# Kernel tuning notes

Measured on AMD Instinct MI355X. Metric: run time of the kernel, lower is better.

## Reference

```python
import jax, jax.numpy as jnp
import numpy as np

B, CIN, H, W = 32, 512, 16, 16
COUT, HEADS, SPARSITY = 2048, 8, 7
D = COUT // HEADS  # 256, must equal H*W
N = H * W


def conv1x1(x, w, b):
    # x: [B,C,H,W], w: [O,C], b: [O]
    return jnp.einsum('bchw,oc->bohw', x, w) + b[None, :, None, None]


def setup_inputs() -> dict:
    key = jax.random.key(0)
    ks = jax.random.split(key, 11)
    def lin(k, o, c):
        bound = 1.0 / np.sqrt(c)
        kw, kb = jax.random.split(k)
        return (jax.random.uniform(kw, (o, c), jnp.float32, -bound, bound),
                jax.random.uniform(kb, (o,), jnp.float32, -bound, bound))
    Wq, bq = lin(ks[0], COUT, CIN)
    Wk, bk = lin(ks[1], COUT, CIN)
    Wv, bv = lin(ks[2], COUT, CIN)
    Wo, bo = lin(ks[3], COUT, COUT)
    # kaiming_uniform_ on [COUT, COUT]
    gain = np.sqrt(2.0) / np.sqrt(5.0)  # default a=sqrt(5)
    bound = gain * np.sqrt(3.0 / COUT)
    coeff = jax.random.uniform(ks[4], (COUT, COUT), jnp.float32, -bound, bound)
    scale = jnp.array([np.sqrt(D)], jnp.float32)
    x = jax.random.normal(ks[5], (B, CIN, H, W), jnp.float32)
    return {"x": x, "Wq": Wq, "bq": bq, "Wk": Wk, "bk": bk, "Wv": Wv,
            "bv": bv, "Wo": Wo, "bo": bo, "coeff": coeff, "scale": scale}


def reference(x, Wq, bq, Wk, bk, Wv, bv, Wo, bo, coeff, scale):
    # enforce_sparsity: keep top-`SPARSITY` |coeff| per row, zero the rest
    _, idx = jax.lax.top_k(jnp.abs(coeff), SPARSITY)  # [COUT, SPARSITY]
    mask = jnp.zeros(coeff.shape, bool).at[jnp.arange(COUT)[:, None], idx].set(True)
    coeff_s = jnp.where(mask, coeff, 0.0)

    q = conv1x1(x, Wq, bq).reshape(B, HEADS, D, N)
    k = conv1x1(x, Wk, bk).reshape(B, HEADS, D, N)
    v = conv1x1(x, Wv, bv).reshape(B, HEADS, D, N)

    attn = jnp.einsum('bhdn,bhdm->bhnm', q, k) / scale[0]  # [B,h,N,N]
    sparse_attn = jnp.einsum('bhnm,mp->bhnp', attn, coeff_s[:D, :D])
    sparse_attn = jax.nn.softmax(sparse_attn, axis=-1)
    out = jnp.einsum('bhnm,bhmd->bhnd', sparse_attn, v.transpose(0, 1, 3, 2))
    out = out.transpose(0, 1, 3, 2).reshape(B, COUT, H, W)
    return conv1x1(out, Wo, bo)
```

## Files before the change

kernel.cpp:

```cpp
#include <hip/hip_runtime.h>

typedef unsigned short ushort;
typedef __attribute__((ext_vector_type(8))) short short8;
typedef __attribute__((ext_vector_type(8))) unsigned short ushort8;
typedef __attribute__((ext_vector_type(4))) unsigned short ushort4v;
typedef __attribute__((ext_vector_type(4))) float fx4;

#define MAXNNZ (256*7)

__device__ __forceinline__ ushort f2bf(float f) {
    union { float f; unsigned u; } v; v.f = f;
    unsigned r = v.u + 0x7fffu + ((v.u >> 16) & 1u);
    return (ushort)(r >> 16);
}

__device__ __forceinline__ float bf2f(ushort b) {
    union { unsigned u; float f; } v; v.u = ((unsigned)b) << 16;
    return v.f;
}

__device__ __forceinline__ void gload_lds16(const ushort* g, ushort* l) {
    __builtin_amdgcn_global_load_lds(
        (const __attribute__((address_space(1))) unsigned int*)g,
        (__attribute__((address_space(3))) unsigned int*)l, 16, 0, 0);
}

__global__ __launch_bounds__(256)
void topk_kernel(const float* __restrict__ coeff,
                 int* __restrict__ coo_cnt, int* __restrict__ coo_m,
                 int* __restrict__ coo_p, float* __restrict__ coo_v)
{
    int row = blockIdx.x;
    int tid = threadIdx.x;
    const float* crow = coeff + (long)row * 2048;
    float av[8];
#pragma unroll
    for (int i = 0; i < 8; ++i) av[i] = fabsf(crow[tid + 256 * i]);
    __shared__ unsigned long long red[256];
    for (int t = 0; t < 7; ++t) {
        float mx = -1.f; int mi = 0;
#pragma unroll
        for (int i = 0; i < 8; ++i) if (av[i] > mx) { mx = av[i]; mi = i; }
        unsigned col = (unsigned)(tid + 256 * mi);
        unsigned long long pk = ((unsigned long long)__float_as_uint(mx) << 32)
                              | (unsigned long long)(2048u - col);
        red[tid] = pk; __syncthreads();
        for (int s = 128; s > 0; s >>= 1) {
            if (tid < s) { if (red[tid + s] > red[tid]) red[tid] = red[tid + s]; }
            __syncthreads();
        }
        unsigned long long w = red[0];
        __syncthreads();
        unsigned wcol = 2048u - (unsigned)(w & 0xffffffffu);
        if ((wcol & 255u) == (unsigned)tid) av[wcol >> 8] = -1.f;
        if (tid == 0 && wcol < 256u) {
            int pos = atomicAdd(coo_cnt, 1);
            coo_m[pos] = row; coo_p[pos] = (int)wcol; coo_v[pos] = crow[wcol];
        }
    }
}

__global__ __launch_bounds__(256)
void csc_kernel(const int* __restrict__ coo_cnt, const int* __restrict__ coo_m,
                const int* __restrict__ coo_p, const float* __restrict__ coo_v,
                int* __restrict__ csc_ptr, int* __restrict__ csc_m,
                float* __restrict__ csc_v, float* __restrict__ csum)
{
    __shared__ int cnt[256];
    __shared__ int off[257];
    __shared__ int cur[256];
    int tid = threadIdx.x;
    cnt[tid] = 0;
    __syncthreads();
    int n = *coo_cnt; if (n > MAXNNZ) n = MAXNNZ;
    for (int e = tid; e < n; e += 256) atomicAdd(&cnt[coo_p[e]], 1);
    __syncthreads();
    if (tid == 0) {
        int s = 0;
        for (int p = 0; p < 256; ++p) { off[p] = s; s += cnt[p]; }
        off[256] = s;
    }
    __syncthreads();
    csc_ptr[tid] = off[tid];
    if (tid == 0) csc_ptr[256] = off[256];
    cur[tid] = off[tid];
    __syncthreads();
    for (int e = tid; e < n; e += 256) {
        int p = coo_p[e];
        int pos = atomicAdd(&cur[p], 1);
        csc_m[pos] = coo_m[e];
        csc_v[pos] = coo_v[e];
    }
    __syncthreads();
    {
        float s = 0.f;
        int e0 = off[tid], e1 = off[tid] + cnt[tid];
        for (int e = e0; e < e1; ++e) s += csc_v[e];
        csum[tid] = s;
    }
}

__global__ void cvt4_kernel(const float* a0, ushort* d0, int n0,
                            const float* a1, ushort* d1, int n1,
                            const float* a2, ushort* d2, int n2,
                            const float* a3, ushort* d3, int n3)
{
    const float* s; ushort* d; int n;
    switch (blockIdx.y) {
        case 0: s = a0; d = d0; n = n0; break;
        case 1: s = a1; d = d1; n = n1; break;
        case 2: s = a2; d = d2; n = n2; break;
        default: s = a3; d = d3; n = n3; break;
    }
    int nv = n >> 2;
    for (int i = blockIdx.x * blockDim.x + threadIdx.x; i < nv; i += gridDim.x * blockDim.x) {
        fx4 v = ((const fx4*)s)[i];
        ushort4v o;
        o[0] = f2bf(v[0]); o[1] = f2bf(v[1]); o[2] = f2bf(v[2]); o[3] = f2bf(v[3]);
        ((ushort4v*)d)[i] = o;
    }
}

__global__ __launch_bounds__(256)
void transpose_f32_bf16(const float* __restrict__ in, ushort* __restrict__ out, int R, int C)
{
    int z = blockIdx.z;
    const float* ib = in + (long)z * R * C;
    ushort* ob = out + (long)z * R * C;
    __shared__ ushort tile[64][72];
    int r0 = blockIdx.x * 64, c0 = blockIdx.y * 64;
    int tid = threadIdx.x;
    int rl = tid >> 2, sg = tid & 3;
#pragma unroll
    for (int h = 0; h < 4; ++h) {
        fx4 v = *(const fx4*)(ib + (long)(r0 + rl) * C + c0 + h * 16 + sg * 4);
#pragma unroll
        for (int i = 0; i < 4; ++i) tile[h * 16 + sg * 4 + i][rl] = f2bf(v[i]);
    }
    __syncthreads();
    int cl = rl;
#pragma unroll
    for (int h = 0; h < 2; ++h) {
        ushort8 vv = *(const ushort8*)(&tile[cl][h * 32 + sg * 8]);
        *(ushort8*)(ob + (long)(c0 + cl) * R + r0 + h * 32 + sg * 8) = vv;
    }
}

__global__ __launch_bounds__(256)
void xcomb_kernel(const ushort* __restrict__ xT, ushort* __restrict__ xc,
                  const int* __restrict__ csc_ptr, const int* __restrict__ csc_m,
                  const float* __restrict__ csc_v)
{
    int b = blockIdx.y;
    int tid = threadIdx.x;
    int p = blockIdx.x * 32 + (tid >> 3);
    int c0 = (tid & 7) * 64;
    const ushort* src = xT + (long)b * 131072;
    float acc[64];
#pragma unroll
    for (int i = 0; i < 64; ++i) acc[i] = 0.f;
    int e0 = csc_ptr[p], e1 = csc_ptr[p + 1];
    for (int e = e0; e < e1; ++e) {
        const ushort* row = src + csc_m[e] * 512 + c0;
        float c = csc_v[e];
#pragma unroll
        for (int u = 0; u < 8; ++u) {
            ushort8 v = *(const ushort8*)(row + u * 8);
#pragma unroll
            for (int t = 0; t < 8; ++t) acc[u * 8 + t] += bf2f(v[t]) * c;
        }
    }
    ushort* dst = xc + (long)b * 131072 + (long)p * 512 + c0;
#pragma unroll
    for (int u = 0; u < 8; ++u) {
        ushort8 o;
#pragma unroll
        for (int t = 0; t < 8; ++t) o[t] = f2bf(acc[u * 8 + t]);
        *(ushort8*)(dst + u * 8) = o;
    }
}

__global__ __launch_bounds__(256, 2)
void attn_kernel(const ushort* __restrict__ Q, const ushort* __restrict__ Kt,
                 const ushort* __restrict__ V, ushort* __restrict__ O,
                 const float* __restrict__ scale_src)
{
    __shared__ __align__(16) ushort PQ[32768];
    __shared__ float rmax[4][128];
    __shared__ float rsum[4][128];

    int bid = blockIdx.x;
    int hf = bid >> 8, z = bid & 255;
    int b = z >> 3, h = z & 7;
    const ushort* Qz = Q + (long)z * 65536 + (long)hf * 32768;
    const ushort* Kz = Kt + (long)z * 65536;
    const ushort* Vz = V + (long)b * 524288 + (long)h * 65536;
    ushort* Ob = O + (long)b * 524288 + (long)h * 256 + (long)hf * 128 * 2048;

    int tid = threadIdx.x;
    int wave = tid >> 6, lane = tid & 63;
    int l16 = lane & 15, quad = lane >> 4;
    int key = l16 & 7;

    {
        int rb = wave * 2 + (lane >> 5);
        const ushort* qsrc = Qz + (long)rb * 256 + (((lane & 31) ^ (rb & 7)) * 8);
        ushort* qdst = PQ + wave * 512;
#pragma unroll
        for (int g = 0; g < 16; ++g)
            gload_lds16(qsrc + g * 2048, qdst + g * 2048);
    }

    const ushort* kfp = Kz + (long)(wave * 64 + l16) * 256 + quad * 8;
    const ushort* vfp = Vz + (long)(wave * 64 + l16) * 256 + quad * 8;

    fx4 acc[8][4];
#pragma unroll
    for (int i = 0; i < 8; ++i)
#pragma unroll
        for (int j = 0; j < 4; ++j) acc[i][j] = (fx4){0.f, 0.f, 0.f, 0.f};

    short8 bfn[4];
#pragma unroll
    for (int j = 0; j < 4; ++j) bfn[j] = *(const short8*)(kfp + j * 4096);

    __syncthreads();

    float sc = 1.0f / scale_src[0];

#pragma unroll
    for (int kd = 0; kd < 8; ++kd) {
        short8 bf[4];
#pragma unroll
        for (int j = 0; j < 4; ++j) bf[j] = bfn[j];
        if (kd < 7) {
#pragma unroll
            for (int j = 0; j < 4; ++j)
                bfn[j] = *(const short8*)(kfp + j * 4096 + (kd + 1) * 32);
        }
        short8 af[8];
#pragma unroll
        for (int i = 0; i < 8; ++i)
            af[i] = *(const short8*)(PQ + (i * 16 + l16) * 256 + (((kd * 4 + quad) ^ key) * 8));
        __builtin_amdgcn_s_setprio(1);
#pragma unroll
        for (int i = 0; i < 8; ++i)
#pragma unroll
            for (int j = 0; j < 4; ++j)
                acc[i][j] = __builtin_amdgcn_mfma_f32_16x16x32_bf16(af[i], bf[j], acc[i][j], 0, 0, 0);
        __builtin_amdgcn_s_setprio(0);
    }

#pragma unroll
    for (int i = 0; i < 8; ++i)
#pragma unroll
        for (int j = 0; j < 4; ++j)
#pragma unroll
            for (int r = 0; r < 4; ++r) acc[i][j][r] *= sc;

    float lm[8][4];
#pragma unroll
    for (int i = 0; i < 8; ++i)
#pragma unroll
        for (int r = 0; r < 4; ++r) {
            float m = -1e30f;
#pragma unroll
            for (int j = 0; j < 4; ++j) m = fmaxf(m, acc[i][j][r]);
            lm[i][r] = m;
        }
#pragma unroll
    for (int d = 1; d < 16; d <<= 1)
#pragma unroll
        for (int i = 0; i < 8; ++i)
#pragma unroll
            for (int r = 0; r < 4; ++r) lm[i][r] = fmaxf(lm[i][r], __shfl_xor(lm[i][r], d, 16));
    if (l16 == 0) {
#pragma unroll
        for (int i = 0; i < 8; ++i)
#pragma unroll
            for (int r = 0; r < 4; ++r)
                rmax[wave][i * 16 + quad * 4 + r] = lm[i][r];
    }
    __syncthreads();

    float ls[8][4];
#pragma unroll
    for (int i = 0; i < 8; ++i)
#pragma unroll
        for (int r = 0; r < 4; ++r) {
            int row = i * 16 + quad * 4 + r;
            float M = fmaxf(fmaxf(rmax[0][row], rmax[1][row]),
                            fmaxf(rmax[2][row], rmax[3][row]));
            float s = 0.f;
#pragma unroll
            for (int j = 0; j < 4; ++j) {
                float e = __expf(acc[i][j][r] - M);
                acc[i][j][r] = e;
                s += e;
            }
            ls[i][r] = s;
        }
#pragma unroll
    for (int d = 1; d < 16; d <<= 1)
#pragma unroll
        for (int i = 0; i < 8; ++i)
#pragma unroll
            for (int r = 0; r < 4; ++r) ls[i][r] += __shfl_xor(ls[i][r], d, 16);
    if (l16 == 0) {
#pragma unroll
        for (int i = 0; i < 8; ++i)
#pragma unroll
            for (int r = 0; r < 4; ++r)
                rsum[wave][i * 16 + quad * 4 + r] = ls[i][r];
    }
    __syncthreads();

    short8 vfn[4];
#pragma unroll
    for (int j = 0; j < 4; ++j) vfn[j] = *(const short8*)(vfp + j * 4096);

#pragma unroll
    for (int i = 0; i < 8; ++i)
#pragma unroll
        for (int r = 0; r < 4; ++r) {
            int row = i * 16 + quad * 4 + r;
            float inv = 1.0f / (rsum[0][row] + rsum[1][row] + rsum[2][row] + rsum[3][row]);
            int k2 = row & 7;
#pragma unroll
            for (int j = 0; j < 4; ++j) {
                int p = wave * 64 + j * 16 + l16;
                PQ[row * 256 + ((((p >> 3) ^ k2) << 3) | (p & 7))] = f2bf(acc[i][j][r] * inv);
            }
        }
    __syncthreads();

    fx4 acc2[8][4];
#pragma unroll
    for (int i = 0; i < 8; ++i)
#pragma unroll
        for (int j = 0; j < 4; ++j) acc2[i][j] = (fx4){0.f, 0.f, 0.f, 0.f};

#pragma unroll
    for (int kp = 0; kp < 8; ++kp) {
        short8 vf[4];
#pragma unroll
        for (int j = 0; j < 4; ++j) vf[j] = vfn[j];
        if (kp < 7) {
#pragma unroll
            for (int j = 0; j < 4; ++j)
                vfn[j] = *(const short8*)(vfp + j * 4096 + (kp + 1) * 32);
        }
        short8 pa[8];
#pragma unroll
        for (int i = 0; i < 8; ++i)
            pa[i] = *(const short8*)(PQ + (i * 16 + l16) * 256 + (((kp * 4 + quad) ^ key) * 8));
        __builtin_amdgcn_s_setprio(1);
#pragma unroll
        for (int i = 0; i < 8; ++i)
#pragma unroll
            for (int j = 0; j < 4; ++j)
                acc2[i][j] = __builtin_amdgcn_mfma_f32_16x16x32_bf16(pa[i], vf[j], acc2[i][j], 0, 0, 0);
        __builtin_amdgcn_s_setprio(0);
    }

    __syncthreads();
#pragma unroll
    for (int i = 0; i < 8; ++i)
#pragma unroll
        for (int j = 0; j < 4; ++j) {
            int rowb = i * 16 + quad * 4;
            int col = wave * 64 + j * 16 + l16;
#pragma unroll
            for (int rr = 0; rr < 4; ++rr) {
                int row = rowb + rr;
                PQ[row * 256 + ((((col >> 3) ^ (row & 7)) << 3) | (col & 7))]
                    = f2bf(acc2[i][j][rr]);
            }
        }
    __syncthreads();
#pragma unroll
    for (int pass = 0; pass < 16; ++pass) {
        int row = pass * 8 + (tid >> 5), ch = tid & 31;
        ushort8 vv = *(const ushort8*)(PQ + row * 256 + ((ch ^ (row & 7)) << 3));
        *(ushort8*)(Ob + (long)row * 2048 + ch * 8) = vv;
    }
}

template<int MODE>
__global__ __launch_bounds__(512, 2)
void gemm256(const ushort* __restrict__ A, const ushort* __restrict__ B,
             const ushort* __restrict__ B2, void* __restrict__ C,
             ushort* __restrict__ Kout,
             const float* __restrict__ bias0, const float* __restrict__ bias1,
             const float* __restrict__ bias2, const float* __restrict__ csum,
             int MT, int K)
{
    __shared__ __align__(16) ushort lds[4][2][8192];

    int nwg = gridDim.x;
    int bid = blockIdx.x;
    int mt, nt;
    if (MODE == 4) {
        int xcd = bid & 7, idx = bid >> 3;
        mt = (xcd & 1) * 12 + idx % 12;
        nt = (xcd >> 1) * 8 + idx / 12;
    } else {
        int cpx = nwg >> 3;
        int swz = (bid & 7) * cpx + (bid >> 3);
        mt = swz % MT; nt = swz / MT;
    }
    int m0 = mt << 8, n0 = nt << 8;
    int sec = m0 >> 11;

    int tid = threadIdx.x;
    int wave = tid >> 6, lane = tid & 63;
    int wr = wave >> 2, wc = wave & 3;
    int l16 = lane & 15, quad = lane >> 4;

    const ushort* Bb = (MODE == 4 && sec == 1) ? B2 : B;

    int lc = (((lane & 3) ^ ((lane >> 3) & 3))) * 8;
    const ushort* gA0 = A + (long long)(m0 + wave * 16 + (lane >> 2)) * K + lc;
    const ushort* gA1 = gA0 + (long long)128 * K;
    const ushort* gB0 = Bb + (long long)(n0 + wave * 16 + (lane >> 2)) * K + lc;
    const ushort* gB1 = gB0 + (long long)128 * K;
    int ldso = wave * 512;

    int rsw = ((l16 >> 1) & 3) * 8;
    int aoff = (wr * 128 + l16) * 32 + ((quad * 8) ^ rsw);
    int boff = (wc * 64 + l16) * 32 + ((quad * 8) ^ rsw);

    fx4 acc[8][4];
#pragma unroll
    for (int i = 0; i < 8; ++i)
#pragma unroll
        for (int j = 0; j < 4; ++j) acc[i][j] = (fx4){0.f, 0.f, 0.f, 0.f};

    auto stageA = [&](int b, int kc) {
        gload_lds16(gA0 + kc, &lds[b][0][ldso]);
        gload_lds16(gA1 + kc, &lds[b][0][4096 + ldso]);
    };
    auto stageB = [&](int b, int kc) {
        gload_lds16(gB0 + kc, &lds[b][1][ldso]);
        gload_lds16(gB1 + kc, &lds[b][1][4096 + ldso]);
    };

    short8 af[4], bf[4];
    auto readA = [&](int b, int half) {
        const ushort* p = &lds[b][0][aoff + half * 2048];
#pragma unroll
        for (int i = 0; i < 4; ++i) af[i] = *(const short8*)(p + i * 512);
    };
    auto readB = [&](int b) {
        const ushort* p = &lds[b][1][boff];
#pragma unroll
        for (int j = 0; j < 4; ++j) bf[j] = *(const short8*)(p + j * 512);
    };
    auto mma = [&](int half) {
        __builtin_amdgcn_s_setprio(1);
#pragma unroll
        for (int i = 0; i < 4; ++i)
#pragma unroll
            for (int j = 0; j < 4; ++j)
                acc[half * 4 + i][j] =
                    __builtin_amdgcn_mfma_f32_16x16x32_bf16(af[i], bf[j], acc[half * 4 + i][j], 0, 0, 0);
        __builtin_amdgcn_s_setprio(0);
    };

    int NT = K >> 5;
    stageA(0, 0);  stageB(0, 0);
    stageA(1, 32); stageB(1, 32);
    stageA(2, 64); stageB(2, 64);
    asm volatile("s_waitcnt vmcnt(8)" ::: "memory");
    __builtin_amdgcn_s_barrier();

    for (int t = 0; t < NT; ++t) {
        int b = t & 3;
        readA(b, 0); readB(b);
        if (t + 3 < NT) stageA((t + 3) & 3, (t + 3) << 5);
        __builtin_amdgcn_s_barrier();
        asm volatile("s_waitcnt lgkmcnt(0)" ::: "memory");
        __builtin_amdgcn_sched_barrier(0);
        mma(0);
        __builtin_amdgcn_s_barrier();
        readA(b, 1);
        if (t + 3 < NT) {
            stageB((t + 3) & 3, (t + 3) << 5);
            asm volatile("s_waitcnt vmcnt(8)" ::: "memory");
        } else if (t + 2 < NT) {
            asm volatile("s_waitcnt vmcnt(4)" ::: "memory");
        } else if (t + 1 < NT) {
            asm volatile("s_waitcnt vmcnt(0)" ::: "memory");
        }
        __builtin_amdgcn_s_barrier();
        asm volatile("s_waitcnt lgkmcnt(0)" ::: "memory");
        __builtin_amdgcn_sched_barrier(0);
        mma(1);
        __builtin_amdgcn_s_barrier();
    }

    if (MODE == 5) {
        float* Cf = (float*)C + (long long)nt * 524288;
#pragma unroll
        for (int i = 0; i < 8; ++i) {
            int m = m0 + wr * 128 + i * 16 + quad * 4;
#pragma unroll
            for (int j = 0; j < 4; ++j) {
                int n = wc * 64 + j * 16 + l16;
                float* dst = Cf + (long long)m * 256 + n;
#pragma unroll
                for (int r = 0; r < 4; ++r)
                    dst[(long)r * 256] = acc[i][j][r] + bias0[m + r];
            }
        }
        return;
    }

    if (MODE == 4) {
        int ms0 = m0 & 2047;
        ushort* ct = &lds[0][0][0];
        if (sec < 2) {
            const float* bs = (sec == 0) ? bias0 : bias1;
            ushort* base = ((sec == 0) ? (ushort*)C : Kout)
                         + (long long)nt * 524288 + (long long)(ms0 >> 8) * 65536;
#pragma unroll
            for (int hh = 0; hh < 2; ++hh) {
                if ((wc >> 1) == hh) {
#pragma unroll
                    for (int i = 0; i < 8; ++i)
#pragma unroll
                        for (int j = 0; j < 4; ++j) {
                            int nl = (wc & 1) * 64 + j * 16 + l16;
                            int ml = wr * 128 + i * 16 + quad * 4;
                            float csf = (sec == 1) ? csum[hh * 128 + nl] : 1.0f;
                            ushort4v pk;
#pragma unroll
                            for (int r = 0; r < 4; ++r)
                                pk[r] = f2bf(acc[i][j][r] + bs[ms0 + ml + r] * csf);
                            *(ushort4v*)(ct + nl * 264 + ml) = pk;
                        }
                }
                __syncthreads();
                int row = tid & 127, c0 = (tid >> 7) * 64;
                ushort* dst = base + (long long)(hh * 128 + row) * 256 + c0;
                const ushort* src = ct + row * 264 + c0;
#pragma unroll
                for (int u = 0; u < 8; ++u)
                    *(ushort8*)(dst + u * 8) = *(const ushort8*)(src + u * 8);
                __syncthreads();
            }
        } else {
            ushort* base = (ushort*)C + 33554432LL + (long long)nt * 524288
                         + (long long)ms0 * 256;
#pragma unroll
            for (int hh = 0; hh < 2; ++hh) {
                if (wr == hh) {
#pragma unroll
                    for (int i = 0; i < 8; ++i)
#pragma unroll
                        for (int j = 0; j < 4; ++j) {
                            int nl = wc * 64 + j * 16 + l16;
                            int ml = i * 16 + quad * 4;
#pragma unroll
                            for (int r = 0; r < 4; ++r)
                                ct[(ml + r) * 264 + nl] =
                                    f2bf(acc[i][j][r] + bias2[ms0 + hh * 128 + ml + r]);
                        }
                }
                __syncthreads();
                int row = tid & 127, c0 = (tid >> 7) * 64;
                ushort* dst = base + (long long)(hh * 128 + row) * 256 + c0;
                const ushort* src = ct + row * 264 + c0;
#pragma unroll
                for (int u = 0; u < 8; ++u)
                    *(ushort8*)(dst + u * 8) = *(const ushort8*)(src + u * 8);
                __syncthreads();
            }
        }
        return;
    }
}

extern "C" void kernel_launch(void* const* d_in, const int* in_sizes, int n_in,
                              void* d_out, int out_size, void* d_ws, size_t ws_size,
                              hipStream_t stream)
{
    const float* x     = (const float*)d_in[0];
    const float* Wq    = (const float*)d_in[1];
    const float* bq    = (const float*)d_in[2];
    const float* Wk    = (const float*)d_in[3];
    const float* bk    = (const float*)d_in[4];
    const float* Wv    = (const float*)d_in[5];
    const float* bv    = (const float*)d_in[6];
    const float* Wo    = (const float*)d_in[7];
    const float* bo    = (const float*)d_in[8];
    const float* coeff = (const float*)d_in[9];
    const float* scale = (const float*)d_in[10];
    float* out = (float*)d_out;

    size_t o = 0;
    char* w = (char*)d_ws;
    auto take = [&](size_t bytes) -> void* {
        void* p = w + o; o += (bytes + 255) & ~(size_t)255; return p;
    };
    int*    coo_cnt = (int*)take(4);
    int*    coo_m   = (int*)take(MAXNNZ * 4);
    int*    coo_p   = (int*)take(MAXNNZ * 4);
    float*  coo_v   = (float*)take(MAXNNZ * 4);
    int*    csc_ptr = (int*)take(257 * 4);
    int*    csc_m   = (int*)take(MAXNNZ * 4);
    float*  csc_v   = (float*)take(MAXNNZ * 4);
    float*  csum    = (float*)take(256 * 4);
    ushort* wqkv = (ushort*)take(6144L * 512 * 2);
    ushort* wob  = (ushort*)take(2048L * 2048 * 2);
    ushort* xT   = (ushort*)take(32L * 256 * 512 * 2);
    ushort* qkv  = (ushort*)take(3 * 16777216L * 2);
    ushort* qbT = qkv;
    ushort* mid = qkv + 16777216L;
    ushort* vb  = qkv + 33554432L;
    ushort* ktc = (ushort*)take(16777216L * 2);
    ushort* xc  = mid;
    ushort* obT = mid;
    (void)in_sizes; (void)n_in; (void)out_size; (void)ws_size;

    hipMemsetAsync(coo_cnt, 0, 4, stream);
    topk_kernel<<<256, 256, 0, stream>>>(coeff, coo_cnt, coo_m, coo_p, coo_v);
    csc_kernel<<<1, 256, 0, stream>>>(coo_cnt, coo_m, coo_p, coo_v,
                                      csc_ptr, csc_m, csc_v, csum);

    cvt4_kernel<<<dim3(1024, 4, 1), 256, 0, stream>>>(
        Wq, wqkv, 2048 * 512, Wk, wqkv + 2048L * 512, 2048 * 512,
        Wv, wqkv + 4096L * 512, 2048 * 512, Wo, wob, 2048 * 2048);
    transpose_f32_bf16<<<dim3(8, 4, 32), 256, 0, stream>>>(x, xT, 512, 256);

    xcomb_kernel<<<dim3(8, 32), 256, 0, stream>>>(xT, xc, csc_ptr, csc_m, csc_v);

    gemm256<4><<<dim3(768, 1, 1), dim3(512, 1, 1), 0, stream>>>(
        wqkv, xT, xc, qkv, ktc, bq, bk, bv, csum, 24, 512);

    attn_kernel<<<512, 256, 0, stream>>>(qbT, ktc, vb, obT, scale);

    gemm256<5><<<dim3(256, 1, 1), dim3(512, 1, 1), 0, stream>>>(
        wob, obT, nullptr, out, nullptr, bo, nullptr, nullptr, nullptr, 8, 2048);
}
```

Measured before the change: 364.2 us.

## Store K and V in 8-element column-blocked layout for coalesced MFMA operand loads

The projection epilogue now writes K and V in a blocked layout where each 8-element chunk of a row is grouped by chunk index across rows (stride 2048). The attention kernel's per-lane K and V fragment loads are changed to match, so the 16 lanes of a quad read consecutive 16-byte chunks instead of rows strided by 512 bytes. The aim is better coalescing of the global loads feeding the MFMAs. The trade-off is that the epilogue stores become strided, 16 bytes every 4 KB, which may cost write efficiency.

```diff
diff --git a/kernel.cpp b/kernel.cpp
--- a/kernel.cpp
+++ b/kernel.cpp
@@ -211,8 +211,9 @@
             gload_lds16(qsrc + g * 2048, qdst + g * 2048);
     }
 
-    const ushort* kfp = Kz + (long)(wave * 64 + l16) * 256 + quad * 8;
-    const ushort* vfp = Vz + (long)(wave * 64 + l16) * 256 + quad * 8;
+    int lrow = wave * 64 + l16;
+    const ushort* kfp = Kz + quad * 2048 + (long)lrow * 8;
+    const ushort* vfp = Vz + quad * 2048 + (long)lrow * 8;
 
     fx4 acc[8][4];
 #pragma unroll
@@ -222,7 +223,7 @@
 
     short8 bfn[4];
 #pragma unroll
-    for (int j = 0; j < 4; ++j) bfn[j] = *(const short8*)(kfp + j * 4096);
+    for (int j = 0; j < 4; ++j) bfn[j] = *(const short8*)(kfp + j * 128);
 
     __syncthreads();
 
@@ -236,7 +237,7 @@
         if (kd < 7) {
 #pragma unroll
             for (int j = 0; j < 4; ++j)
-                bfn[j] = *(const short8*)(kfp + j * 4096 + (kd + 1) * 32);
+                bfn[j] = *(const short8*)(kfp + (kd + 1) * 8192 + j * 128);
         }
         short8 af[8];
 #pragma unroll
@@ -317,7 +318,7 @@
 
     short8 vfn[4];
 #pragma unroll
-    for (int j = 0; j < 4; ++j) vfn[j] = *(const short8*)(vfp + j * 4096);
+    for (int j = 0; j < 4; ++j) vfn[j] = *(const short8*)(vfp + j * 128);
 
 #pragma unroll
     for (int i = 0; i < 8; ++i)
@@ -348,7 +349,7 @@
         if (kp < 7) {
 #pragma unroll
             for (int j = 0; j < 4; ++j)
-                vfn[j] = *(const short8*)(vfp + j * 4096 + (kp + 1) * 32);
+                vfn[j] = *(const short8*)(vfp + (kp + 1) * 8192 + j * 128);
         }
         short8 pa[8];
 #pragma unroll
@@ -521,8 +522,11 @@
         ushort* ct = &lds[0][0][0];
         if (sec < 2) {
             const float* bs = (sec == 0) ? bias0 : bias1;
-            ushort* base = ((sec == 0) ? (ushort*)C : Kout)
-                         + (long long)nt * 524288 + (long long)(ms0 >> 8) * 65536;
+            ushort* base;
+            if (sec == 0)
+                base = (ushort*)C + (long long)nt * 524288 + (long long)(ms0 >> 8) * 65536;
+            else
+                base = Kout + (long long)(nt * 8 + (ms0 >> 8)) * 65536;
 #pragma unroll
             for (int hh = 0; hh < 2; ++hh) {
                 if ((wc >> 1) == hh) {
@@ -542,16 +546,24 @@
                 }
                 __syncthreads();
                 int row = tid & 127, c0 = (tid >> 7) * 64;
-                ushort* dst = base + (long long)(hh * 128 + row) * 256 + c0;
                 const ushort* src = ct + row * 264 + c0;
-#pragma unroll
-                for (int u = 0; u < 8; ++u)
-                    *(ushort8*)(dst + u * 8) = *(const ushort8*)(src + u * 8);
+                if (sec == 0) {
+                    ushort* dst = base + (long long)(hh * 128 + row) * 256 + c0;
+#pragma unroll
+                    for (int u = 0; u < 8; ++u)
+                        *(ushort8*)(dst + u * 8) = *(const ushort8*)(src + u * 8);
+                } else {
+                    ushort* pdst = base + (long long)(hh * 128 + row) * 8;
+#pragma unroll
+                    for (int u = 0; u < 8; ++u)
+                        *(ushort8*)(pdst + (long long)((c0 >> 3) + u) * 2048)
+                            = *(const ushort8*)(src + u * 8);
+                }
                 __syncthreads();
             }
         } else {
-            ushort* base = (ushort*)C + 33554432LL + (long long)nt * 524288
-                         + (long long)ms0 * 256;
+            ushort* vbase = (ushort*)C + 33554432LL + (long long)nt * 524288
+                          + (long long)(ms0 >> 8) * 65536;
 #pragma unroll
             for (int hh = 0; hh < 2; ++hh) {
                 if (wr == hh) {
@@ -569,11 +581,12 @@
                 }
                 __syncthreads();
                 int row = tid & 127, c0 = (tid >> 7) * 64;
-                ushort* dst = base + (long long)(hh * 128 + row) * 256 + c0;
                 const ushort* src = ct + row * 264 + c0;
+                ushort* pdst = vbase + (long long)(hh * 128 + row) * 8;
 #pragma unroll
                 for (int u = 0; u < 8; ++u)
-                    *(ushort8*)(dst + u * 8) = *(const ushort8*)(src + u * 8);
+                    *(ushort8*)(pdst + (long long)((c0 >> 3) + u) * 2048)
+                        = *(const ushort8*)(src + u * 8);
                 __syncthreads();
             }
         }
```

Result: no change. 358.9 us (-1.5%).
